# Kernel tuning notes

Measured on AMD Instinct MI355X. Metric: run time of the kernel, lower is better.

The kernel has to match this reference:

```python
import jax, jax.numpy as jnp
import numpy as np

N_NODES = 100000
N_EDGES = 1600000
IN_C = 128
HID_C = 64
HEADS = 2
OUT_C = 40
NEG_SLOPE = 0.2  # PyG GATConv default


def setup_inputs() -> dict:
    key = jax.random.key(0)
    ks = jax.random.split(key, 10)
    x = jax.random.normal(ks[0], (N_NODES, IN_C), dtype=jnp.float32)
    edge_index = jax.random.randint(ks[1], (2, N_EDGES), 0, N_NODES, dtype=jnp.int32)
    # layer 1 params: Linear(in, heads*hid), att_src/att_dst [heads, hid], bias [heads*hid]
    s1 = 1.0 / np.sqrt(IN_C)
    W1 = jax.random.uniform(ks[2], (IN_C, HEADS * HID_C), minval=-s1, maxval=s1, dtype=jnp.float32)
    att_src1 = jax.random.normal(ks[3], (HEADS, HID_C), dtype=jnp.float32) * 0.1
    att_dst1 = jax.random.normal(ks[4], (HEADS, HID_C), dtype=jnp.float32) * 0.1
    b1 = jnp.zeros((HEADS * HID_C,), dtype=jnp.float32)
    # layer 2 params: Linear(heads*hid, out), heads=1, concat=False
    s2 = 1.0 / np.sqrt(HEADS * HID_C)
    W2 = jax.random.uniform(ks[5], (HEADS * HID_C, OUT_C), minval=-s2, maxval=s2, dtype=jnp.float32)
    att_src2 = jax.random.normal(ks[6], (1, OUT_C), dtype=jnp.float32) * 0.1
    att_dst2 = jax.random.normal(ks[7], (1, OUT_C), dtype=jnp.float32) * 0.1
    b2 = jnp.zeros((OUT_C,), dtype=jnp.float32)
    return {"x": x, "edge_index": edge_index, "W1": W1, "att_src1": att_src1,
            "att_dst1": att_dst1, "b1": b1, "W2": W2, "att_src2": att_src2,
            "att_dst2": att_dst2, "b2": b2}


def _gat_conv(x, src, dst, n, W, a_src, a_dst):
    # x: [N, F_in]; W: [F_in, H*C]; a_src/a_dst: [H, C]
    H, C = a_src.shape
    h = (x @ W).reshape(n, H, C)                       # [N, H, C]
    alpha_src = jnp.einsum('nhc,hc->nh', h, a_src)     # [N, H]
    alpha_dst = jnp.einsum('nhc,hc->nh', h, a_dst)
    e = alpha_src[src] + alpha_dst[dst]                # [E, H]
    e = jax.nn.leaky_relu(e, NEG_SLOPE)
    # numerically stable softmax over edges grouped by destination node
    m = jax.ops.segment_max(e, dst, num_segments=n)    # [N, H]
    ex = jnp.exp(e - m[dst])
    s = jax.ops.segment_sum(ex, dst, num_segments=n)
    coef = ex / (s[dst] + 1e-16)                       # [E, H]
    msg = h[src] * coef[:, :, None]                    # [E, H, C]
    return jax.ops.segment_sum(msg, dst, num_segments=n)  # [N, H, C]


def reference(x, edge_index, W1, att_src1, att_dst1, b1, W2, att_src2, att_dst2, b2):
    n = x.shape[0]
    # PyG GATConv adds self-loops by default
    loops = jnp.arange(n, dtype=edge_index.dtype)
    src = jnp.concatenate([edge_index[0], loops])
    dst = jnp.concatenate([edge_index[1], loops])
    # layer 1: heads=2, concat -> [N, H*C] + bias, then ELU
    h1 = _gat_conv(x, src, dst, n, W1, att_src1, att_dst1)
    h1 = h1.reshape(n, -1) + b1
    h1 = jax.nn.elu(h1)
    # layer 2: heads=1, concat=False -> mean over heads (=squeeze) + bias
    h2 = _gat_conv(h1, src, dst, n, W2, att_src2, att_dst2)
    h2 = h2.mean(axis=1) + b2
    return jax.nn.log_softmax(h2, axis=1)
```

## Files before the change

kernel.cpp:

```cpp
#include <hip/hip_runtime.h>
#include <hip/hip_fp16.h>
#include <math.h>

#define N_NODES 100000
#define N_EDGES 1600000
#define E_TOT   (N_EDGES + N_NODES)

#define NB     512
#define NPB    196
#define BCAP   4096
#define BIN_CH 4096
#define NBIN_WG ((E_TOT + BIN_CH - 1) / BIN_CH)

__device__ __forceinline__ float wexp(float v) {
    v = v > 0.f ? v : 0.2f * v;
    return __expf(v);
}

__global__ __launch_bounds__(256) void gemm1_k(
    const float* __restrict__ x, const float* __restrict__ W1,
    const float* __restrict__ as1, const float* __restrict__ ad1,
    __half* __restrict__ h1h, float* __restrict__ asrc, float* __restrict__ adst)
{
    __shared__ float xs[64][65];
    __shared__ float Wsh[64][128];
    const int t = threadIdx.x;
    const int nbase = blockIdx.x * 64;
    const int c4 = t & 31;
    const int ng = t >> 5;

    float acc[8][4];
#pragma unroll
    for (int i = 0; i < 8; ++i)
#pragma unroll
        for (int j = 0; j < 4; ++j) acc[i][j] = 0.f;

    for (int kt = 0; kt < 128; kt += 64) {
        __syncthreads();
        {
            int r = t >> 4;
            int c = (t & 15) * 4;
#pragma unroll
            for (int p = 0; p < 4; ++p) {
                int row = p * 16 + r;
                int gr = nbase + row; if (gr > N_NODES - 1) gr = N_NODES - 1;
                float4 v = *(const float4*)(x + (size_t)gr * 128 + kt + c);
                xs[row][c + 0] = v.x; xs[row][c + 1] = v.y;
                xs[row][c + 2] = v.z; xs[row][c + 3] = v.w;
            }
        }
        {
            int r = t >> 5;
            int c = (t & 31) * 4;
#pragma unroll
            for (int p = 0; p < 8; ++p) {
                int row = p * 8 + r;
                *(float4*)&Wsh[row][c] = *(const float4*)(W1 + (size_t)(kt + row) * 128 + c);
            }
        }
        __syncthreads();

#pragma unroll 4
        for (int k = 0; k < 64; ++k) {
            float4 w = *(const float4*)&Wsh[k][c4 * 4];
            float x0 = xs[ng * 8 + 0][k], x1 = xs[ng * 8 + 1][k];
            float x2 = xs[ng * 8 + 2][k], x3 = xs[ng * 8 + 3][k];
            float x4 = xs[ng * 8 + 4][k], x5 = xs[ng * 8 + 5][k];
            float x6 = xs[ng * 8 + 6][k], x7 = xs[ng * 8 + 7][k];
            acc[0][0] += x0 * w.x; acc[0][1] += x0 * w.y; acc[0][2] += x0 * w.z; acc[0][3] += x0 * w.w;
            acc[1][0] += x1 * w.x; acc[1][1] += x1 * w.y; acc[1][2] += x1 * w.z; acc[1][3] += x1 * w.w;
            acc[2][0] += x2 * w.x; acc[2][1] += x2 * w.y; acc[2][2] += x2 * w.z; acc[2][3] += x2 * w.w;
            acc[3][0] += x3 * w.x; acc[3][1] += x3 * w.y; acc[3][2] += x3 * w.z; acc[3][3] += x3 * w.w;
            acc[4][0] += x4 * w.x; acc[4][1] += x4 * w.y; acc[4][2] += x4 * w.z; acc[4][3] += x4 * w.w;
            acc[5][0] += x5 * w.x; acc[5][1] += x5 * w.y; acc[5][2] += x5 * w.z; acc[5][3] += x5 * w.w;
            acc[6][0] += x6 * w.x; acc[6][1] += x6 * w.y; acc[6][2] += x6 * w.z; acc[6][3] += x6 * w.w;
            acc[7][0] += x7 * w.x; acc[7][1] += x7 * w.y; acc[7][2] += x7 * w.z; acc[7][3] += x7 * w.w;
        }
    }

    float4 as4 = ((const float4*)as1)[c4];
    float4 ad4 = ((const float4*)ad1)[c4];
#pragma unroll
    for (int i = 0; i < 8; ++i) {
        int node = nbase + ng * 8 + i;
        float ax = acc[i][0], ay = acc[i][1], az = acc[i][2], aw = acc[i][3];
        if (node < N_NODES) {
            __half2* row = (__half2*)(h1h + (size_t)node * 128);
            row[2 * c4]     = __floats2half2_rn(ax, ay);
            row[2 * c4 + 1] = __floats2half2_rn(az, aw);
        }
        float ps = ax * as4.x + ay * as4.y + az * as4.z + aw * as4.w;
        float pd = ax * ad4.x + ay * ad4.y + az * ad4.z + aw * ad4.w;
#pragma unroll
        for (int off = 1; off < 16; off <<= 1) {
            ps += __shfl_xor(ps, off);
            pd += __shfl_xor(pd, off);
        }
        if ((t & 15) == 0 && node < N_NODES) {
            int h = c4 >> 4;
            asrc[node * 2 + h] = ps;
            adst[node * 2 + h] = pd;
        }
    }
}

__global__ __launch_bounds__(256) void bin_k(
    const int* __restrict__ ei, int* __restrict__ bcur, unsigned* __restrict__ bdata)
{
    __shared__ int hist[NB];
    __shared__ int base[NB];
    const int t = threadIdx.x;
    const int e0 = blockIdx.x * BIN_CH;
    const int n = min(BIN_CH, E_TOT - e0);

    for (int b = t; b < NB; b += 256) hist[b] = 0;
    __syncthreads();

    for (int i = t; i < n; i += 256) {
        int e = e0 + i;
        int d = (e < N_EDGES) ? ei[N_EDGES + e] : e - N_EDGES;
        atomicAdd(&hist[d / NPB], 1);
    }
    __syncthreads();

    for (int b = t; b < NB; b += 256) {
        int c = hist[b];
        base[b] = c ? atomicAdd(&bcur[b], c) : 0;
        hist[b] = 0;
    }
    __syncthreads();

    for (int i = t; i < n; i += 256) {
        int e = e0 + i;
        int s, d;
        if (e < N_EDGES) { s = ei[e]; d = ei[N_EDGES + e]; }
        else             { s = d = e - N_EDGES; }
        int b  = d / NPB;
        int dl = d - b * NPB;
        int pos = base[b] + atomicAdd(&hist[b], 1);
        if (pos < BCAP)
            bdata[(size_t)b * BCAP + pos] = (unsigned)s | ((unsigned)dl << 17);
    }
}

__global__ __launch_bounds__(512) void scanb_k(
    const int* __restrict__ bcur, int* __restrict__ bbase)
{
    __shared__ int a[NB], b_[NB];
    int t = threadIdx.x;
    int v = bcur[t];
    a[t] = v;
    __syncthreads();
    int* src = a; int* dst = b_;
    for (int off = 1; off < NB; off <<= 1) {
        dst[t] = (t >= off) ? src[t - off] + src[t] : src[t];
        __syncthreads();
        int* tmp = src; src = dst; dst = tmp;
    }
    bbase[t] = src[t] - v;
}

__global__ __launch_bounds__(256) void build_k(
    const unsigned* __restrict__ bdata, const int* __restrict__ bcur,
    const int* __restrict__ bbase, int* __restrict__ row_start,
    int* __restrict__ csr_src)
{
    __shared__ unsigned rec[BCAP];
    __shared__ int hist[256];
    __shared__ int excl[NPB];
    __shared__ int lcur[NPB];
    const int t = threadIdx.x;
    const int b = blockIdx.x;
    const int cnt = min(bcur[b], BCAP);
    const int bb = bbase[b];

    hist[t] = 0;
    if (t < NPB) lcur[t] = 0;
    __syncthreads();

    for (int i = t; i < cnt; i += 256) {
        unsigned r = bdata[(size_t)b * BCAP + i];
        rec[i] = r;
        atomicAdd(&hist[r >> 17], 1);
    }
    __syncthreads();

    int v = hist[t];
    __syncthreads();
    for (int off = 1; off < 256; off <<= 1) {
        int y = (t >= off) ? hist[t - off] : 0;
        __syncthreads();
        hist[t] += y;
        __syncthreads();
    }
    if (t < NPB) excl[t] = hist[t] - v;
    __syncthreads();

    int node = b * NPB + t;
    if (t < NPB && node <= N_NODES) row_start[node] = bb + excl[t];

    for (int i = t; i < cnt; i += 256) {
        unsigned r = rec[i];
        int dl = r >> 17;
        int s  = r & 0x1FFFF;
        int slot = atomicAdd(&lcur[dl], 1);
        csr_src[bb + excl[dl] + slot] = s;
    }
}

__global__ __launch_bounds__(256) void fagg1_k(
    const int* __restrict__ csr_src, const int* __restrict__ row_start,
    const float* __restrict__ asrc, const float* __restrict__ adst,
    const __half* __restrict__ h1h, const float* __restrict__ b1,
    __half* __restrict__ out1h)
{
    int node = blockIdx.x * 4 + (threadIdx.x >> 6);
    int L = threadIdx.x & 63;
    int h = L >> 5;
    int b = row_start[node], e = row_start[node + 1];
    const float* as_h = asrc + h;
    float ad = adst[node * 2 + h];
    const __half2* H = (const __half2*)h1h;

    float2 a0 = make_float2(0.f, 0.f), a1 = a0, a2 = a0, a3 = a0;
    float d0 = 0.f, d1 = 0.f, d2 = 0.f, d3 = 0.f;

    int j = b;
    for (; j + 3 < e; j += 4) {
        int s0 = csr_src[j], s1 = csr_src[j + 1], s2 = csr_src[j + 2], s3 = csr_src[j + 3];
        float w0 = wexp(as_h[s0 * 2] + ad);
        float w1 = wexp(as_h[s1 * 2] + ad);
        float w2 = wexp(as_h[s2 * 2] + ad);
        float w3 = wexp(as_h[s3 * 2] + ad);
        float2 x0 = __half22float2(H[(size_t)s0 * 64 + L]);
        float2 x1 = __half22float2(H[(size_t)s1 * 64 + L]);
        float2 x2 = __half22float2(H[(size_t)s2 * 64 + L]);
        float2 x3 = __half22float2(H[(size_t)s3 * 64 + L]);
        a0.x += w0 * x0.x; a0.y += w0 * x0.y; d0 += w0;
        a1.x += w1 * x1.x; a1.y += w1 * x1.y; d1 += w1;
        a2.x += w2 * x2.x; a2.y += w2 * x2.y; d2 += w2;
        a3.x += w3 * x3.x; a3.y += w3 * x3.y; d3 += w3;
    }
    for (; j < e; ++j) {
        int s = csr_src[j];
        float w = wexp(as_h[s * 2] + ad);
        float2 xv = __half22float2(H[(size_t)s * 64 + L]);
        a0.x += w * xv.x; a0.y += w * xv.y; d0 += w;
    }

    float inv = 1.f / (((d0 + d1) + (d2 + d3)) + 1e-16f);
    float2 bb = ((const float2*)b1)[L];
    float vx = (a0.x + a1.x + a2.x + a3.x) * inv + bb.x;
    float vy = (a0.y + a1.y + a2.y + a3.y) * inv + bb.y;
    vx = vx > 0.f ? vx : expm1f(vx);
    vy = vy > 0.f ? vy : expm1f(vy);
    ((__half2*)(out1h + (size_t)node * 128))[L] = __floats2half2_rn(vx, vy);
}

__global__ __launch_bounds__(256) void gemm2_k(
    const __half* __restrict__ in1h, const float* __restrict__ W2,
    const float* __restrict__ as2, const float* __restrict__ ad2,
    __half* __restrict__ h2h, float* __restrict__ asrc, float* __restrict__ adst)
{
    __shared__ float xs[64][65];
    __shared__ float Wsh[64][64];
    __shared__ float as_s[64], ad_s[64];
    const int t = threadIdx.x;
    const int nbase = blockIdx.x * 64;
    const int c4 = t & 15;
    const int ng = t >> 4;

    if (t < 64) {
        as_s[t] = (t < 40) ? as2[t] : 0.f;
        ad_s[t] = (t < 40) ? ad2[t] : 0.f;
    }

    float acc[4][4];
#pragma unroll
    for (int i = 0; i < 4; ++i)
#pragma unroll
        for (int j = 0; j < 4; ++j) acc[i][j] = 0.f;

    for (int kt = 0; kt < 128; kt += 64) {
        __syncthreads();
        {
            int r = t >> 4;
            int c = (t & 15) * 4;
#pragma unroll
            for (int p = 0; p < 4; ++p) {
                int row = p * 16 + r;
                int gr = nbase + row; if (gr > N_NODES - 1) gr = N_NODES - 1;
                const __half2* src = (const __half2*)(in1h + (size_t)gr * 128 + kt + c);
                float2 f01 = __half22float2(src[0]);
                float2 f23 = __half22float2(src[1]);
                xs[row][c + 0] = f01.x; xs[row][c + 1] = f01.y;
                xs[row][c + 2] = f23.x; xs[row][c + 3] = f23.y;
            }
        }
        for (int i = t; i < 4096; i += 256) {
            int k = i >> 6, c = i & 63;
            Wsh[k][c] = (c < 40) ? W2[(size_t)(kt + k) * 40 + c] : 0.f;
        }
        __syncthreads();

#pragma unroll 4
        for (int k = 0; k < 64; ++k) {
            float4 w = *(const float4*)&Wsh[k][c4 * 4];
            float x0 = xs[ng * 4 + 0][k], x1 = xs[ng * 4 + 1][k];
            float x2 = xs[ng * 4 + 2][k], x3 = xs[ng * 4 + 3][k];
            acc[0][0] += x0 * w.x; acc[0][1] += x0 * w.y; acc[0][2] += x0 * w.z; acc[0][3] += x0 * w.w;
            acc[1][0] += x1 * w.x; acc[1][1] += x1 * w.y; acc[1][2] += x1 * w.z; acc[1][3] += x1 * w.w;
            acc[2][0] += x2 * w.x; acc[2][1] += x2 * w.y; acc[2][2] += x2 * w.z; acc[2][3] += x2 * w.w;
            acc[3][0] += x3 * w.x; acc[3][1] += x3 * w.y; acc[3][2] += x3 * w.z; acc[3][3] += x3 * w.w;
        }
    }

    float4 as4 = *(const float4*)&as_s[c4 * 4];
    float4 ad4 = *(const float4*)&ad_s[c4 * 4];
#pragma unroll
    for (int i = 0; i < 4; ++i) {
        int node = nbase + ng * 4 + i;
        float ax = acc[i][0], ay = acc[i][1], az = acc[i][2], aw = acc[i][3];
        if (node < N_NODES) {
            __half2* row = (__half2*)(h2h + (size_t)node * 64);
            row[2 * c4]     = __floats2half2_rn(ax, ay);
            row[2 * c4 + 1] = __floats2half2_rn(az, aw);
        }
        float ps = ax * as4.x + ay * as4.y + az * as4.z + aw * as4.w;
        float pd = ax * ad4.x + ay * ad4.y + az * ad4.z + aw * ad4.w;
#pragma unroll
        for (int off = 1; off < 16; off <<= 1) {
            ps += __shfl_xor(ps, off);
            pd += __shfl_xor(pd, off);
        }
        if ((t & 15) == 0 && node < N_NODES) {
            asrc[node] = ps;
            adst[node] = pd;
        }
    }
}

__global__ __launch_bounds__(256) void fagg2_k(
    const int* __restrict__ csr_src, const int* __restrict__ row_start,
    const float* __restrict__ asrc, const float* __restrict__ adst,
    const __half* __restrict__ h2h, const float* __restrict__ b2,
    float* __restrict__ out)
{
    int node = blockIdx.x * 4 + (threadIdx.x >> 6);
    int L = threadIdx.x & 63;
    bool act = L < 40;
    int col = act ? L : 0;
    int b = row_start[node], e = row_start[node + 1];
    float ad = adst[node];

    float a0 = 0.f, a1 = 0.f, a2 = 0.f, a3 = 0.f;
    float d0 = 0.f, d1 = 0.f, d2 = 0.f, d3 = 0.f;

    int j = b;
    for (; j + 3 < e; j += 4) {
        int s0 = csr_src[j], s1 = csr_src[j + 1], s2 = csr_src[j + 2], s3 = csr_src[j + 3];
        float w0 = wexp(asrc[s0] + ad);
        float w1 = wexp(asrc[s1] + ad);
        float w2 = wexp(asrc[s2] + ad);
        float w3 = wexp(asrc[s3] + ad);
        float x0 = __half2float(h2h[(size_t)s0 * 64 + col]);
        float x1 = __half2float(h2h[(size_t)s1 * 64 + col]);
        float x2 = __half2float(h2h[(size_t)s2 * 64 + col]);
        float x3 = __half2float(h2h[(size_t)s3 * 64 + col]);
        a0 += w0 * x0; d0 += w0;
        a1 += w1 * x1; d1 += w1;
        a2 += w2 * x2; d2 += w2;
        a3 += w3 * x3; d3 += w3;
    }
    for (; j < e; ++j) {
        int s = csr_src[j];
        float w = wexp(asrc[s] + ad);
        float xv = __half2float(h2h[(size_t)s * 64 + col]);
        a0 += w * xv; d0 += w;
    }

    float den = (d0 + d1) + (d2 + d3);
    float acc = (a0 + a1) + (a2 + a3);
    float v = act ? acc / (den + 1e-16f) + b2[L] : -1e30f;
    float mx = v;
#pragma unroll
    for (int off = 32; off; off >>= 1) mx = fmaxf(mx, __shfl_xor(mx, off));
    float ex = act ? __expf(v - mx) : 0.f;
#pragma unroll
    for (int off = 32; off; off >>= 1) ex += __shfl_xor(ex, off);
    if (act) out[(size_t)node * 40 + L] = v - mx - logf(ex);
}

extern "C" void kernel_launch(void* const* d_in, const int* in_sizes, int n_in,
                              void* d_out, int out_size, void* d_ws, size_t ws_size,
                              hipStream_t stream)
{
    const float* x   = (const float*)d_in[0];
    const int*   ei  = (const int*)d_in[1];
    const float* W1  = (const float*)d_in[2];
    const float* as1 = (const float*)d_in[3];
    const float* ad1 = (const float*)d_in[4];
    const float* b1  = (const float*)d_in[5];
    const float* W2  = (const float*)d_in[6];
    const float* as2 = (const float*)d_in[7];
    const float* ad2 = (const float*)d_in[8];
    const float* b2  = (const float*)d_in[9];
    float* out = (float*)d_out;

    float* ws = (float*)d_ws;
    __half* h1h   = (__half*)ws;
    __half* out1h = (__half*)(ws + 6400000);
    float* asrc1 = ws + 19200000;
    float* adst1 = ws + 19400000;
    float* asrc2 = ws + 19600000;
    float* adst2 = ws + 19700000;
    int* bcur      = (int*)(ws + 19800000);
    int* bbase     = (int*)(ws + 19801000);
    int* row_start = (int*)(ws + 19802000);
    int* csr_src   = (int*)(ws + 19910000);
    unsigned* bdata = (unsigned*)(ws + 21700000);

    hipMemsetAsync(bcur, 0, NB * sizeof(int), stream);

    bin_k<<<NBIN_WG, 256, 0, stream>>>(ei, bcur, bdata);
    scanb_k<<<1, 512, 0, stream>>>(bcur, bbase);
    build_k<<<NB, 256, 0, stream>>>(bdata, bcur, bbase, row_start, csr_src);

    gemm1_k<<<1563, 256, 0, stream>>>(x, W1, as1, ad1, h1h, asrc1, adst1);
    fagg1_k<<<25000, 256, 0, stream>>>(csr_src, row_start, asrc1, adst1, h1h, b1, out1h);

    __half* h2h = h1h;
    gemm2_k<<<1563, 256, 0, stream>>>(out1h, W2, as2, ad2, h2h, asrc2, adst2);
    fagg2_k<<<25000, 256, 0, stream>>>(csr_src, row_start, asrc2, adst2, h2h, b2, out);
}
```

Before: 301.3 us.

## Use bf16 MFMA for first GEMM and register-cache edges in binning

Layer-1 GEMM now runs on bf16 MFMA 16x16x32 instructions instead of scalar FP32 FMAs through LDS. A separate prep kernel converts x to bf16 and another repacks W1 into the MFMA operand layout. The bin kernel also loads each thread's 16 edges into registers once instead of reading edge_index twice. Workspace offsets move to make room for the new buffers. The extra x conversion pass adds memory traffic and a launch, and bf16 inputs lower GEMM precision.

```diff
diff --git a/kernel.cpp b/kernel.cpp
--- a/kernel.cpp
+++ b/kernel.cpp
@@ -12,94 +12,101 @@
 #define BIN_CH 4096
 #define NBIN_WG ((E_TOT + BIN_CH - 1) / BIN_CH)
 
+typedef __attribute__((ext_vector_type(8))) short short8v;
+typedef __attribute__((ext_vector_type(4))) float float4v;
+
 __device__ __forceinline__ float wexp(float v) {
     v = v > 0.f ? v : 0.2f * v;
     return __expf(v);
 }
 
+__device__ __forceinline__ unsigned short f2bf(float f) {
+    unsigned u = __float_as_uint(f);
+    return (unsigned short)((u + 0x7FFFu + ((u >> 16) & 1u)) >> 16);
+}
+
+__global__ __launch_bounds__(256) void xprep_k(
+    const float* __restrict__ x, unsigned short* __restrict__ xb)
+{
+    int gid = blockIdx.x * 256 + threadIdx.x;
+    float4 v = ((const float4*)x)[gid];
+    ushort4 o;
+    o.x = f2bf(v.x); o.y = f2bf(v.y); o.z = f2bf(v.z); o.w = f2bf(v.w);
+    ((ushort4*)xb)[gid] = o;
+}
+
+__global__ __launch_bounds__(256) void w1prep_k(
+    const float* __restrict__ W1, unsigned short* __restrict__ W1b)
+{
+    for (int idx = threadIdx.x; idx < 16384; idx += 256) {
+        int i    = idx & 7;
+        int lane = (idx >> 3) & 63;
+        int f    = (idx >> 9) & 7;
+        int ks   = idx >> 12;
+        int k   = ks * 32 + (lane >> 4) * 8 + i;
+        int col = f * 16 + (lane & 15);
+        W1b[idx] = f2bf(W1[k * 128 + col]);
+    }
+}
+
 __global__ __launch_bounds__(256) void gemm1_k(
-    const float* __restrict__ x, const float* __restrict__ W1,
+    const unsigned short* __restrict__ xb, const unsigned short* __restrict__ W1b,
     const float* __restrict__ as1, const float* __restrict__ ad1,
     __half* __restrict__ h1h, float* __restrict__ asrc, float* __restrict__ adst)
 {
-    __shared__ float xs[64][65];
-    __shared__ float Wsh[64][128];
     const int t = threadIdx.x;
-    const int nbase = blockIdx.x * 64;
-    const int c4 = t & 31;
-    const int ng = t >> 5;
-
-    float acc[8][4];
-#pragma unroll
-    for (int i = 0; i < 8; ++i)
-#pragma unroll
-        for (int j = 0; j < 4; ++j) acc[i][j] = 0.f;
-
-    for (int kt = 0; kt < 128; kt += 64) {
-        __syncthreads();
-        {
-            int r = t >> 4;
-            int c = (t & 15) * 4;
-#pragma unroll
-            for (int p = 0; p < 4; ++p) {
-                int row = p * 16 + r;
-                int gr = nbase + row; if (gr > N_NODES - 1) gr = N_NODES - 1;
-                float4 v = *(const float4*)(x + (size_t)gr * 128 + kt + c);
-                xs[row][c + 0] = v.x; xs[row][c + 1] = v.y;
-                xs[row][c + 2] = v.z; xs[row][c + 3] = v.w;
-            }
-        }
-        {
-            int r = t >> 5;
-            int c = (t & 31) * 4;
-#pragma unroll
-            for (int p = 0; p < 8; ++p) {
-                int row = p * 8 + r;
-                *(float4*)&Wsh[row][c] = *(const float4*)(W1 + (size_t)(kt + row) * 128 + c);
-            }
-        }
-        __syncthreads();
-
-#pragma unroll 4
-        for (int k = 0; k < 64; ++k) {
-            float4 w = *(const float4*)&Wsh[k][c4 * 4];
-            float x0 = xs[ng * 8 + 0][k], x1 = xs[ng * 8 + 1][k];
-            float x2 = xs[ng * 8 + 2][k], x3 = xs[ng * 8 + 3][k];
-            float x4 = xs[ng * 8 + 4][k], x5 = xs[ng * 8 + 5][k];
-            float x6 = xs[ng * 8 + 6][k], x7 = xs[ng * 8 + 7][k];
-            acc[0][0] += x0 * w.x; acc[0][1] += x0 * w.y; acc[0][2] += x0 * w.z; acc[0][3] += x0 * w.w;
-            acc[1][0] += x1 * w.x; acc[1][1] += x1 * w.y; acc[1][2] += x1 * w.z; acc[1][3] += x1 * w.w;
-            acc[2][0] += x2 * w.x; acc[2][1] += x2 * w.y; acc[2][2] += x2 * w.z; acc[2][3] += x2 * w.w;
-            acc[3][0] += x3 * w.x; acc[3][1] += x3 * w.y; acc[3][2] += x3 * w.z; acc[3][3] += x3 * w.w;
-            acc[4][0] += x4 * w.x; acc[4][1] += x4 * w.y; acc[4][2] += x4 * w.z; acc[4][3] += x4 * w.w;
-            acc[5][0] += x5 * w.x; acc[5][1] += x5 * w.y; acc[5][2] += x5 * w.z; acc[5][3] += x5 * w.w;
-            acc[6][0] += x6 * w.x; acc[6][1] += x6 * w.y; acc[6][2] += x6 * w.z; acc[6][3] += x6 * w.w;
-            acc[7][0] += x7 * w.x; acc[7][1] += x7 * w.y; acc[7][2] += x7 * w.z; acc[7][3] += x7 * w.w;
-        }
-    }
-
-    float4 as4 = ((const float4*)as1)[c4];
-    float4 ad4 = ((const float4*)ad1)[c4];
-#pragma unroll
-    for (int i = 0; i < 8; ++i) {
-        int node = nbase + ng * 8 + i;
-        float ax = acc[i][0], ay = acc[i][1], az = acc[i][2], aw = acc[i][3];
-        if (node < N_NODES) {
-            __half2* row = (__half2*)(h1h + (size_t)node * 128);
-            row[2 * c4]     = __floats2half2_rn(ax, ay);
-            row[2 * c4 + 1] = __floats2half2_rn(az, aw);
-        }
-        float ps = ax * as4.x + ay * as4.y + az * as4.z + aw * as4.w;
-        float pd = ax * ad4.x + ay * ad4.y + az * ad4.z + aw * ad4.w;
+    const int w = t >> 6, L = t & 63;
+    const int lr = L & 15;
+    const int lg = L >> 4;
+    const int nbase = blockIdx.x * 64 + w * 16;
+
+    float4v acc[8];
+#pragma unroll
+    for (int f = 0; f < 8; ++f) acc[f] = (float4v)0.f;
+
+    int arow = nbase + lr; if (arow >= N_NODES) arow = N_NODES - 1;
+    const unsigned short* xrow = xb + (size_t)arow * 128 + lg * 8;
+
+#pragma unroll
+    for (int ks = 0; ks < 4; ++ks) {
+        short8v a = *(const short8v*)(xrow + ks * 32);
+        const unsigned short* wb = W1b + ((size_t)ks * 8 * 64 + L) * 8;
+#pragma unroll
+        for (int f = 0; f < 8; ++f) {
+            short8v b = *(const short8v*)(wb + (size_t)f * 512);
+            acc[f] = __builtin_amdgcn_mfma_f32_16x16x32_bf16(a, b, acc[f], 0, 0, 0);
+        }
+    }
+
+    float as_v[8], ad_v[8];
+#pragma unroll
+    for (int f = 0; f < 8; ++f) {
+        as_v[f] = as1[f * 16 + lr];
+        ad_v[f] = ad1[f * 16 + lr];
+    }
+
+#pragma unroll
+    for (int r = 0; r < 4; ++r) {
+        int node = nbase + lg * 4 + r;
+        bool ok = node < N_NODES;
+        if (ok) {
+#pragma unroll
+            for (int f = 0; f < 8; ++f)
+                h1h[(size_t)node * 128 + f * 16 + lr] = __float2half_rn(acc[f][r]);
+        }
+        float ps0 = 0.f, pd0 = 0.f, ps1 = 0.f, pd1 = 0.f;
+#pragma unroll
+        for (int f = 0; f < 4; ++f) { ps0 += acc[f][r] * as_v[f]; pd0 += acc[f][r] * ad_v[f]; }
+#pragma unroll
+        for (int f = 4; f < 8; ++f) { ps1 += acc[f][r] * as_v[f]; pd1 += acc[f][r] * ad_v[f]; }
 #pragma unroll
         for (int off = 1; off < 16; off <<= 1) {
-            ps += __shfl_xor(ps, off);
-            pd += __shfl_xor(pd, off);
-        }
-        if ((t & 15) == 0 && node < N_NODES) {
-            int h = c4 >> 4;
-            asrc[node * 2 + h] = ps;
-            adst[node * 2 + h] = pd;
+            ps0 += __shfl_xor(ps0, off); pd0 += __shfl_xor(pd0, off);
+            ps1 += __shfl_xor(ps1, off); pd1 += __shfl_xor(pd1, off);
+        }
+        if (lr == 0 && ok) {
+            asrc[node * 2 + 0] = ps0; asrc[node * 2 + 1] = ps1;
+            adst[node * 2 + 0] = pd0; adst[node * 2 + 1] = pd1;
         }
     }
 }
@@ -111,16 +118,23 @@
     __shared__ int base[NB];
     const int t = threadIdx.x;
     const int e0 = blockIdx.x * BIN_CH;
-    const int n = min(BIN_CH, E_TOT - e0);
+
+    int rs[16], rd[16];
+#pragma unroll
+    for (int p = 0; p < 16; ++p) {
+        int e = e0 + p * 256 + t;
+        if (e < E_TOT) {
+            if (e < N_EDGES) { rs[p] = ei[e]; rd[p] = ei[N_EDGES + e]; }
+            else             { rs[p] = rd[p] = e - N_EDGES; }
+        } else rd[p] = -1;
+    }
 
     for (int b = t; b < NB; b += 256) hist[b] = 0;
     __syncthreads();
 
-    for (int i = t; i < n; i += 256) {
-        int e = e0 + i;
-        int d = (e < N_EDGES) ? ei[N_EDGES + e] : e - N_EDGES;
-        atomicAdd(&hist[d / NPB], 1);
-    }
+#pragma unroll
+    for (int p = 0; p < 16; ++p)
+        if (rd[p] >= 0) atomicAdd(&hist[rd[p] / NPB], 1);
     __syncthreads();
 
     for (int b = t; b < NB; b += 256) {
@@ -130,16 +144,14 @@
     }
     __syncthreads();
 
-    for (int i = t; i < n; i += 256) {
-        int e = e0 + i;
-        int s, d;
-        if (e < N_EDGES) { s = ei[e]; d = ei[N_EDGES + e]; }
-        else             { s = d = e - N_EDGES; }
-        int b  = d / NPB;
-        int dl = d - b * NPB;
+#pragma unroll
+    for (int p = 0; p < 16; ++p) {
+        if (rd[p] < 0) continue;
+        int b  = rd[p] / NPB;
+        int dl = rd[p] - b * NPB;
         int pos = base[b] + atomicAdd(&hist[b], 1);
         if (pos < BCAP)
-            bdata[(size_t)b * BCAP + pos] = (unsigned)s | ((unsigned)dl << 17);
+            bdata[(size_t)b * BCAP + pos] = (unsigned)rs[p] | ((unsigned)dl << 17);
     }
 }
 
@@ -320,14 +332,14 @@
 #pragma unroll
     for (int i = 0; i < 4; ++i) {
         int node = nbase + ng * 4 + i;
-        float ax = acc[i][0], ay = acc[i][1], az = acc[i][2], aw = acc[i][3];
+        float axx = acc[i][0], ayy = acc[i][1], azz = acc[i][2], aww = acc[i][3];
         if (node < N_NODES) {
             __half2* row = (__half2*)(h2h + (size_t)node * 64);
-            row[2 * c4]     = __floats2half2_rn(ax, ay);
-            row[2 * c4 + 1] = __floats2half2_rn(az, aw);
-        }
-        float ps = ax * as4.x + ay * as4.y + az * as4.z + aw * as4.w;
-        float pd = ax * ad4.x + ay * ad4.y + az * ad4.z + aw * ad4.w;
+            row[2 * c4]     = __floats2half2_rn(axx, ayy);
+            row[2 * c4 + 1] = __floats2half2_rn(azz, aww);
+        }
+        float ps = axx * as4.x + ayy * as4.y + azz * as4.z + aww * as4.w;
+        float pd = axx * ad4.x + ayy * ad4.y + azz * ad4.z + aww * ad4.w;
 #pragma unroll
         for (int off = 1; off < 16; off <<= 1) {
             ps += __shfl_xor(ps, off);
@@ -414,19 +426,24 @@
     float* adst1 = ws + 19400000;
     float* asrc2 = ws + 19600000;
     float* adst2 = ws + 19700000;
-    int* bcur      = (int*)(ws + 19800000);
-    int* bbase     = (int*)(ws + 19801000);
-    int* row_start = (int*)(ws + 19802000);
-    int* csr_src   = (int*)(ws + 19910000);
-    unsigned* bdata = (unsigned*)(ws + 21700000);
+    int* bcur      = (int*)(ws + 20110000);
+    int* bbase     = (int*)(ws + 20111000);
+    int* row_start = (int*)(ws + 20112000);
+    int* csr_src   = (int*)(ws + 20220000);
+    unsigned* bdata = (unsigned*)(ws + 22000000);
+    unsigned short* xb  = (unsigned short*)(ws + 24100000);
+    unsigned short* W1b = (unsigned short*)(ws + 27300000);
 
     hipMemsetAsync(bcur, 0, NB * sizeof(int), stream);
+
+    xprep_k<<<12500, 256, 0, stream>>>(x, xb);
+    w1prep_k<<<1, 256, 0, stream>>>(W1, W1b);
 
     bin_k<<<NBIN_WG, 256, 0, stream>>>(ei, bcur, bdata);
     scanb_k<<<1, 512, 0, stream>>>(bcur, bbase);
     build_k<<<NB, 256, 0, stream>>>(bdata, bcur, bbase, row_start, csr_src);
 
-    gemm1_k<<<1563, 256, 0, stream>>>(x, W1, as1, ad1, h1h, asrc1, adst1);
+    gemm1_k<<<1563, 256, 0, stream>>>(xb, W1b, as1, ad1, h1h, asrc1, adst1);
     fagg1_k<<<25000, 256, 0, stream>>>(csr_src, row_start, asrc1, adst1, h1h, b1, out1h);
 
     __half* h2h = h1h;
```

Measured after the change: 286.1 us. 1.05x faster.
